# Optimization experiments

Measured on AMD Instinct MI355X. Metric: run time of the kernel, lower is better.

Reference implementation:

```python
import jax, jax.numpy as jnp
import numpy as np

N, E, F, H, C, T = 100000, 1600000, 128, 64, 8, 4

def setup_inputs() -> dict:
    key = jax.random.key(0)
    ks = jax.random.split(key, 16)
    inp = {
        'x': jax.random.normal(ks[0], (N, F), dtype=jnp.float32),
        'node_types': jax.random.randint(ks[1], (N,), 0, T, dtype=jnp.int64),
        'edge_index0': jax.random.randint(ks[2], (2, E), 0, N, dtype=jnp.int64),
        'edge_index1': jax.random.randint(ks[3], (2, E), 0, N, dtype=jnp.int64),
        # per-node-type input projections
        'W_in': jax.random.normal(ks[4], (T, F, H), dtype=jnp.float32) / np.sqrt(F),
        'b_in': jnp.zeros((T, H), dtype=jnp.float32),
        # 4 GCN convs (layer0: paths [0,0],[0,1]; layer1: paths [0,0],[1,0])
        'W_conv': jax.random.normal(ks[5], (4, H, H), dtype=jnp.float32) / np.sqrt(H),
        'b_conv': jnp.zeros((4, H), dtype=jnp.float32),
        # output attention/classifier layers
        'W1': jax.random.normal(ks[6], (H, H), dtype=jnp.float32) / np.sqrt(H),
        'b1': jnp.zeros((H,), dtype=jnp.float32),
        'W2': jax.random.normal(ks[7], (H, 1), dtype=jnp.float32) / np.sqrt(H),
        'b2': jnp.zeros((1,), dtype=jnp.float32),
        'W3': jax.random.normal(ks[8], (H, C), dtype=jnp.float32) / np.sqrt(H),
        'b3': jnp.zeros((C,), dtype=jnp.float32),
    }
    return inp


def gcn_conv(x, edge_index, W, b):
    # PyG GCNConv: add self-loops, symmetric normalization, then scatter-add.
    n = x.shape[0]
    loop = jnp.arange(n, dtype=edge_index.dtype)
    src = jnp.concatenate([edge_index[0], loop])
    dst = jnp.concatenate([edge_index[1], loop])
    deg = jax.ops.segment_sum(jnp.ones_like(dst, dtype=x.dtype), dst, num_segments=n)
    dinv = jnp.where(deg > 0, jax.lax.rsqrt(deg), 0.0)
    norm = dinv[src] * dinv[dst]            # [E+N]
    xw = x @ W                              # [N,H]
    msg = xw[src] * norm[:, None]           # [E+N,H]
    out = jax.ops.segment_sum(msg, dst, num_segments=n)
    return out + b


def reference(x, node_types, edge_index0, edge_index1,
              W_in, b_in, W_conv, b_conv, W1, b1, W2, b2, W3, b3):
    # per-node-type input linear (fixed small loop over T types)
    hid = jnp.zeros((x.shape[0], H), dtype=x.dtype)
    for t in range(T):
        ht = x @ W_in[t] + b_in[t]
        hid = jnp.where((node_types == t)[:, None], ht, hid)
    edges = [edge_index0, edge_index1]
    states = [hid]
    # layer 0: paths [state 0, adj 0], [state 0, adj 1]; layer_agg = max
    h0 = gcn_conv(states[0], edges[0], W_conv[0], b_conv[0])
    h1 = gcn_conv(states[0], edges[1], W_conv[1], b_conv[1])
    states.append(jnp.maximum(h0, h1))
    # layer 1: paths [state 0, adj 0], [state 1, adj 0]
    h2 = gcn_conv(states[0], edges[0], W_conv[2], b_conv[2])
    h3 = gcn_conv(states[1], edges[0], W_conv[3], b_conv[3])
    states.append(jnp.maximum(h2, h3))
    # LayerNorm (no affine) + gelu (torch default = exact erf form)
    tmp = states[-1]
    mu = jnp.mean(tmp, axis=-1, keepdims=True)
    var = jnp.mean(jnp.square(tmp - mu), axis=-1, keepdims=True)
    tmp = (tmp - mu) * jax.lax.rsqrt(var + 1e-5)
    hidi = jax.nn.gelu(tmp, approximate=False)
    # attention combine over (single) temp state
    attn = jax.nn.softmax(jnp.tanh(hidi @ W1 + b1) @ W2 + b2, axis=-1)  # [N,1] -> ones
    out = attn * hidi
    return out @ W3 + b3
```

## Files before the change

kernel.cpp:

```cpp
#include <hip/hip_runtime.h>
#include <hip/hip_bf16.h>
#include <math.h>


#define HID   64
#define RB    128
#define CHUNK 4096

__device__ __forceinline__ float bflo(unsigned u) { return __int_as_float((int)(u << 16)); }
__device__ __forceinline__ float bfhi(unsigned u) { return __int_as_float((int)(u & 0xFFFF0000u)); }
__device__ __forceinline__ float bf2f(ushort v) { return __int_as_float((int)(((unsigned)v) << 16)); }
__device__ __forceinline__ ushort f2bf(float f) {
    unsigned u = __float_as_uint(f);
    unsigned r = u + 0x7FFFu + ((u >> 16) & 1u);
    return (ushort)(r >> 16);
}
__device__ __forceinline__ void addw(float a[4], uint2 v, float wgt) {
    a[0] = fmaf(bflo(v.x), wgt, a[0]);
    a[1] = fmaf(bfhi(v.x), wgt, a[1]);
    a[2] = fmaf(bflo(v.y), wgt, a[2]);
    a[3] = fmaf(bfhi(v.y), wgt, a[3]);
}
__device__ __forceinline__ void addu(float a[4], uint2 v) {
    a[0] += bflo(v.x); a[1] += bfhi(v.x);
    a[2] += bflo(v.y); a[3] += bfhi(v.y);
}

__global__ void zeroRow(unsigned* __restrict__ ghz, unsigned* __restrict__ s1z,
                        float* __restrict__ dinv0, float* __restrict__ dinv1, int N) {
    int tid = threadIdx.x;
    if (tid < 32) { ghz[tid] = 0u; s1z[tid] = 0u; }
    if (tid == 0) { dinv0[N] = 0.0f; dinv1[N] = 0.0f; }
}

__global__ void histA(const int* __restrict__ dst0, const int* __restrict__ dst1,
                      int E, unsigned M, int* __restrict__ bcnt) {
    __shared__ int h[2 * RB];
    for (int i = threadIdx.x; i < 2 * RB; i += blockDim.x) h[i] = 0;
    __syncthreads();
    int stride = gridDim.x * blockDim.x;
    for (int i = blockIdx.x * blockDim.x + threadIdx.x; i < E; i += stride) {
        atomicAdd(&h[__umulhi((unsigned)dst0[i], M)], 1);
        atomicAdd(&h[RB + __umulhi((unsigned)dst1[i], M)], 1);
    }
    __syncthreads();
    for (int i = threadIdx.x; i < 2 * RB; i += blockDim.x)
        if (h[i]) atomicAdd(&bcnt[i], h[i]);
}

__global__ void scanA(const int* __restrict__ bcnt, int* __restrict__ bbase,
                      int* __restrict__ bcur) {
    __shared__ int t[2 * RB];
    int tid = threadIdx.x;
    int orig = bcnt[tid];
    t[tid] = orig;
    __syncthreads();
    int list = tid >> 7, r = tid & (RB - 1);
    for (int o = 1; o < RB; o <<= 1) {
        int u = (r >= o) ? t[tid - o] : 0;
        __syncthreads();
        t[tid] += u;
        __syncthreads();
    }
    int incl = t[tid];
    int excl = incl - orig;
    bbase[list * (RB + 1) + r] = excl;
    bcur[tid] = excl;
    if (r == RB - 1) bbase[list * (RB + 1) + RB] = incl;
}

__global__ void __launch_bounds__(256) partB(const int* __restrict__ e0,
                                             const int* __restrict__ e1,
                                             int E, int BW, unsigned M,
                                             int* __restrict__ bcur_all,
                                             unsigned* __restrict__ arena_all) {
    __shared__ int hist[RB], scn[RB], lbase[RB], cur[RB], gbase[RB];
    __shared__ uint2 buf[CHUNK];
    int half = gridDim.x >> 1;
    int list = (blockIdx.x >= half) ? 1 : 0;
    const int* src = list ? e1 : e0;
    const int* dst = src + E;
    int* bcur = bcur_all + list * RB;
    unsigned* arena = arena_all + (size_t)list * E;
    int blk = blockIdx.x - list * half;
    int tid = threadIdx.x;

    for (int c0 = blk * CHUNK; c0 < E; c0 += half * CHUNK) {
        int cn = min(CHUNK, E - c0);
        for (int i = tid; i < RB; i += 256) hist[i] = 0;
        __syncthreads();
        unsigned ls[16], ld[16];
        #pragma unroll
        for (int k = 0; k < 16; ++k) {
            int j = k * 256 + tid;
            ld[k] = 0xFFFFFFFFu; ls[k] = 0;
            if (j < cn) {
                ls[k] = (unsigned)src[c0 + j];
                ld[k] = (unsigned)dst[c0 + j];
                atomicAdd(&hist[__umulhi(ld[k], M)], 1);
            }
        }
        __syncthreads();
        if (tid < RB) scn[tid] = hist[tid];
        __syncthreads();
        for (int o = 1; o < RB; o <<= 1) {
            int u = (tid < RB && tid >= o) ? scn[tid - o] : 0;
            __syncthreads();
            if (tid < RB) scn[tid] += u;
            __syncthreads();
        }
        if (tid < RB) {
            int ex = scn[tid] - hist[tid];
            lbase[tid] = ex;
            cur[tid]   = ex;
            gbase[tid] = hist[tid] ? atomicAdd(&bcur[tid], hist[tid]) : 0;
        }
        __syncthreads();
        #pragma unroll
        for (int k = 0; k < 16; ++k) {
            if (ld[k] != 0xFFFFFFFFu) {
                int b = __umulhi(ld[k], M);
                int slot = atomicAdd(&cur[b], 1);
                buf[slot] = make_uint2(ls[k], ld[k]);
            }
        }
        __syncthreads();
        for (int i = tid; i < cn; i += 256) {
            uint2 p = buf[i];
            int b = __umulhi(p.y, M);
            arena[gbase[b] + (i - lbase[b])] = (p.x << 10) | (p.y - (unsigned)(b * BW));
        }
        __syncthreads();
    }
}

__global__ void __launch_bounds__(1024) buildC(const unsigned* __restrict__ arena_all,
                                               const int* __restrict__ bbase,
                                               int E, int N, int BW,
                                               int* __restrict__ csr0p, int* __restrict__ csr1p,
                                               unsigned* __restrict__ offp0, unsigned* __restrict__ offp1,
                                               float* __restrict__ dinv0, float* __restrict__ dinv1) {
    __shared__ int degl[800], scn[800], cur[800];
    int list = blockIdx.x >> 7, rb = blockIdx.x & (RB - 1);
    const unsigned* arena = arena_all + (size_t)list * E;
    int* csr = list ? csr1p : csr0p;
    unsigned* offp = list ? offp1 : offp0;
    float* dinv = list ? dinv1 : dinv0;
    int base = bbase[list * (RB + 1) + rb];
    int end  = bbase[list * (RB + 1) + rb + 1];
    int csrb = base + 16 * BW * rb;
    int nbase = rb * BW;
    int nn = min(BW, N - nbase);
    if (nn <= 0) return;
    int tid = threadIdx.x;
    for (int i = tid; i < nn; i += 1024) degl[i] = 0;
    __syncthreads();
    for (int j = base + tid; j < end; j += 1024)
        atomicAdd(&degl[arena[j] & 1023u], 1);
    __syncthreads();
    int d = (tid < nn) ? degl[tid] : 0;
    int dp = d ? ((d + 15) & ~15) : 0;
    if (tid < nn) scn[tid] = dp;
    __syncthreads();
    for (int o = 1; o < nn; o <<= 1) {
        int u = (tid < nn && tid >= o) ? scn[tid - o] : 0;
        __syncthreads();
        if (tid < nn) scn[tid] += u;
        __syncthreads();
    }
    if (tid < nn) {
        int ex = scn[tid] - dp;
        cur[tid] = ex;
        offp[nbase + tid] = (unsigned)(csrb + ex) | ((unsigned)(dp >> 4) << 25);
        dinv[nbase + tid] = rsqrtf((float)(d + 1));
        for (int j = ex + d; j < ex + dp; ++j) csr[csrb + j] = N;
    }
    __syncthreads();
    for (int j = base + tid; j < end; j += 1024) {
        unsigned p = arena[j];
        int loc = atomicAdd(&cur[p & 1023u], 1);
        csr[csrb + loc] = (int)(p >> 10);
    }
}

__global__ void input_proj(const float* __restrict__ x, const int* __restrict__ types,
                           const float* __restrict__ W_in, const float* __restrict__ b_in,
                           ushort* __restrict__ gh, int N, int F) {
    __shared__ float xs[4 * 128];
    int tid = threadIdx.x;
    int w = tid >> 6, h = tid & 63;
    int n0 = blockIdx.x * 4;
    for (int i = tid; i < 4 * F; i += 256) {
        int nn = n0 + i / F;
        xs[i] = (nn < N) ? x[(size_t)nn * F + (i % F)] : 0.0f;
    }
    __syncthreads();
    int n = n0 + w;
    if (n >= N) return;
    int t = types[n];
    const float* W = W_in + (size_t)t * F * HID;
    float acc = b_in[t * HID + h];
    const float* xr = xs + w * F;
    #pragma unroll 16
    for (int f = 0; f < F; ++f)
        acc = fmaf(xr[f], W[(size_t)f * HID + h], acc);
    gh[(size_t)n * HID + h] = f2bf(acc);
}

__device__ __forceinline__ void gatherW(const uint2* __restrict__ GH,
                                        const float* __restrict__ dv,
                                        const int* __restrict__ csr,
                                        unsigned wword, int q, int fl, float a[4]) {
    int base = (int)(wword & 0x1FFFFFFu);
    int it = (int)(wword >> 25);
    if (it == 0) return;
    const int* cp = csr + base;
    int ia = cp[q], ib = cp[4 + q], ic = cp[8 + q], id = cp[12 + q];
    while (true) {
        uint2 va = GH[(size_t)ia * 16 + fl];
        uint2 vb = GH[(size_t)ib * 16 + fl];
        uint2 vc = GH[(size_t)ic * 16 + fl];
        uint2 vd = GH[(size_t)id * 16 + fl];
        float wa = dv[ia], wb = dv[ib], wc = dv[ic], wd = dv[id];
        --it; cp += 16;
        int na = 0, nb = 0, nc = 0, nd = 0;
        if (it > 0) { na = cp[q]; nb = cp[4 + q]; nc = cp[8 + q]; nd = cp[12 + q]; }
        addw(a, va, wa); addw(a, vb, wb); addw(a, vc, wc); addw(a, vd, wd);
        if (it == 0) break;
        ia = na; ib = nb; ic = nc; id = nd;
    }
}

__device__ __forceinline__ void gatherU(const uint2* __restrict__ GH,
                                        const int* __restrict__ csr,
                                        unsigned wword, int q, int fl, float a[4]) {
    int base = (int)(wword & 0x1FFFFFFu);
    int it = (int)(wword >> 25);
    if (it == 0) return;
    const int* cp = csr + base;
    int ia = cp[q], ib = cp[4 + q], ic = cp[8 + q], id = cp[12 + q];
    while (true) {
        uint2 va = GH[(size_t)ia * 16 + fl];
        uint2 vb = GH[(size_t)ib * 16 + fl];
        uint2 vc = GH[(size_t)ic * 16 + fl];
        uint2 vd = GH[(size_t)id * 16 + fl];
        --it; cp += 16;
        int na = 0, nb = 0, nc = 0, nd = 0;
        if (it > 0) { na = cp[q]; nb = cp[4 + q]; nc = cp[8 + q]; nd = cp[12 + q]; }
        addu(a, va); addu(a, vb); addu(a, vc); addu(a, vd);
        if (it == 0) break;
        ia = na; ib = nb; ic = nc; id = nd;
    }
}

__global__ void __launch_bounds__(512) gatherL1(
        const ushort* __restrict__ gh,
        const unsigned* __restrict__ offp0, const int* __restrict__ csr0p,
        const float* __restrict__ dinv0,
        const unsigned* __restrict__ offp1, const int* __restrict__ csr1p,
        const float* __restrict__ dinv1,
        const float* __restrict__ W_conv, const float* __restrict__ b_conv,
        unsigned* __restrict__ a0g, ushort* __restrict__ s1g, int N) {
    __shared__ float Ws[2 * HID * HID];
    __shared__ float l0[8][HID], l1[8][HID];
    int tid = threadIdx.x;
    for (int i = tid; i < 2 * HID * HID; i += 512) Ws[i] = W_conv[i];
    __syncthreads();
    int w = tid >> 6, lane = tid & 63;
    int q = lane >> 4, fl = lane & 15;
    int n = blockIdx.x * 8 + w;
    if (n >= N) return;
    const uint2* GH = (const uint2*)gh;
    float d0 = dinv0[n], d1 = dinv1[n];
    float a0[4] = {0, 0, 0, 0}, a1[4] = {0, 0, 0, 0};
    if (q == 0) {
        uint2 sv = GH[(size_t)n * 16 + fl];
        float f0 = bflo(sv.x), f1 = bfhi(sv.x), f2 = bflo(sv.y), f3 = bfhi(sv.y);
        a0[0] = f0 * d0; a0[1] = f1 * d0; a0[2] = f2 * d0; a0[3] = f3 * d0;
        a1[0] = f0 * d1; a1[1] = f1 * d1; a1[2] = f2 * d1; a1[3] = f3 * d1;
    }
    gatherW(GH, dinv0, csr0p, offp0[n], q, fl, a0);
    gatherW(GH, dinv1, csr1p, offp1[n], q, fl, a1);
    #pragma unroll
    for (int k = 0; k < 4; ++k) {
        a0[k] += __shfl_xor(a0[k], 16, 64);
        a0[k] += __shfl_xor(a0[k], 32, 64);
        a1[k] += __shfl_xor(a1[k], 16, 64);
        a1[k] += __shfl_xor(a1[k], 32, 64);
        a0[k] *= d0;
        a1[k] *= d1;
    }
    if (q == 0) {
        *(float4*)&l0[w][fl * 4] = make_float4(a0[0], a0[1], a0[2], a0[3]);
        *(float4*)&l1[w][fl * 4] = make_float4(a1[0], a1[1], a1[2], a1[3]);
        uint2 pk;
        pk.x = (unsigned)f2bf(a0[0]) | ((unsigned)f2bf(a0[1]) << 16);
        pk.y = (unsigned)f2bf(a0[2]) | ((unsigned)f2bf(a0[3]) << 16);
        ((uint2*)a0g)[(size_t)n * 16 + fl] = pk;
    }
    int h = lane;
    float m0 = b_conv[h];
    float m1 = b_conv[HID + h];
    #pragma unroll 8
    for (int k = 0; k < HID; ++k) {
        m0 = fmaf(l0[w][k], Ws[k * HID + h], m0);
        m1 = fmaf(l1[w][k], Ws[HID * HID + k * HID + h], m1);
    }
    s1g[(size_t)n * HID + h] = f2bf(fmaxf(m0, m1) * d0);
}

__global__ void __launch_bounds__(512) gatherL2(
        const unsigned* __restrict__ a0g, const ushort* __restrict__ s1g,
        const unsigned* __restrict__ offp0, const int* __restrict__ csr0p,
        const float* __restrict__ dinv0,
        const float* __restrict__ W_conv, const float* __restrict__ b_conv,
        const float* __restrict__ W3, const float* __restrict__ b3,
        float* __restrict__ out, int N) {
    __shared__ float Ws[2 * HID * HID];
    __shared__ float W3s[HID * 8];
    __shared__ float l2[8][HID], l3[8][HID], gs[8][HID];
    int tid = threadIdx.x;
    for (int i = tid; i < 2 * HID * HID; i += 512) Ws[i] = W_conv[2 * HID * HID + i];
    if (tid < HID * 8) W3s[tid] = W3[tid];
    __syncthreads();
    int w = tid >> 6, lane = tid & 63;
    int q = lane >> 4, fl = lane & 15;
    int n = blockIdx.x * 8 + w;
    if (n >= N) return;
    const uint2* S = (const uint2*)s1g;
    float d0 = dinv0[n];
    float a[4] = {0, 0, 0, 0};
    if (q == 0) {
        uint2 sv = S[(size_t)n * 16 + fl];
        a[0] = bflo(sv.x); a[1] = bfhi(sv.x);
        a[2] = bflo(sv.y); a[3] = bfhi(sv.y);
        uint2 av = ((const uint2*)a0g)[(size_t)n * 16 + fl];
        *(float4*)&l2[w][fl * 4] = make_float4(bflo(av.x), bfhi(av.x), bflo(av.y), bfhi(av.y));
    }
    gatherU(S, csr0p, offp0[n], q, fl, a);
    #pragma unroll
    for (int k = 0; k < 4; ++k) {
        a[k] += __shfl_xor(a[k], 16, 64);
        a[k] += __shfl_xor(a[k], 32, 64);
        a[k] *= d0;
    }
    if (q == 0)
        *(float4*)&l3[w][fl * 4] = make_float4(a[0], a[1], a[2], a[3]);
    int h = lane;
    float m2 = b_conv[2 * HID + h];
    float m3 = b_conv[3 * HID + h];
    #pragma unroll 8
    for (int k = 0; k < HID; ++k) {
        m2 = fmaf(l2[w][k], Ws[k * HID + h], m2);
        m3 = fmaf(l3[w][k], Ws[HID * HID + k * HID + h], m3);
    }
    float s2 = fmaxf(m2, m3);
    float sum = s2;
    #pragma unroll
    for (int off = 32; off; off >>= 1) sum += __shfl_xor(sum, off, 64);
    float mu = sum * (1.0f / 64.0f);
    float dv = s2 - mu;
    float v = dv * dv;
    #pragma unroll
    for (int off = 32; off; off >>= 1) v += __shfl_xor(v, off, 64);
    float xn = dv * rsqrtf(v * (1.0f / 64.0f) + 1e-5f);
    float g = 0.5f * xn * (1.0f + erff(xn * 0.70710678118654752f));
    gs[w][h] = g;
    if (h < 8) {
        float acc = b3[h];
        #pragma unroll 8
        for (int k = 0; k < HID; ++k)
            acc = fmaf(gs[w][k], W3s[k * 8 + h], acc);
        out[(size_t)n * 8 + h] = acc;
    }
}

extern "C" void kernel_launch(void* const* d_in, const int* in_sizes, int n_in,
                              void* d_out, int out_size, void* d_ws, size_t ws_size,
                              hipStream_t stream) {
    const float* x          = (const float*)d_in[0];
    const int*   node_types = (const int*)d_in[1];
    const int*   e0         = (const int*)d_in[2];
    const int*   e1         = (const int*)d_in[3];
    const float* W_in       = (const float*)d_in[4];
    const float* b_in       = (const float*)d_in[5];
    const float* W_conv     = (const float*)d_in[6];
    const float* b_conv     = (const float*)d_in[7];
    const float* W3         = (const float*)d_in[12];
    const float* b3         = (const float*)d_in[13];
    float* out = (float*)d_out;

    int N = in_sizes[1];
    int F = in_sizes[0] / N;
    int E = in_sizes[2] / 2;
    int BW = (N + RB - 1) / RB;
    unsigned M = (unsigned)(0x100000000ULL / (unsigned long long)BW) + 1u;
    size_t EP = (size_t)E + 16 * (size_t)BW * RB + 64;

    unsigned* ws32 = (unsigned*)d_ws;
    int*      bcnt  = (int*)ws32;
    int*      bbase = bcnt + 2 * RB;
    int*      bcur  = bbase + 2 * (RB + 1);
    unsigned* offp0 = (unsigned*)(bcur + 2 * RB + 6);
    unsigned* offp1 = offp0 + (N + 1);
    float*    dinv0 = (float*)(offp1 + (N + 1));
    float*    dinv1 = dinv0 + (N + 1);
    int*      csr0p = (int*)(dinv1 + (N + 1));
    int*      csr1p = csr0p + EP;
    ushort*   gh    = (ushort*)(csr1p + EP);
    ushort*   s1g   = gh + (size_t)(N + 1) * HID;
    unsigned* a0g   = (unsigned*)(s1g + (size_t)(N + 1) * HID);
    unsigned* arena = a0g;

    (void)hipMemsetAsync(bcnt, 0, 2 * RB * sizeof(int), stream);
    zeroRow<<<1, 64, 0, stream>>>((unsigned*)(gh + (size_t)N * HID),
                                  (unsigned*)(s1g + (size_t)N * HID), dinv0, dinv1, N);
    histA<<<1024, 256, 0, stream>>>(e0 + E, e1 + E, E, M, bcnt);
    scanA<<<1, 256, 0, stream>>>(bcnt, bbase, bcur);
    partB<<<256, 256, 0, stream>>>(e0, e1, E, BW, M, bcur, arena);
    buildC<<<2 * RB, 1024, 0, stream>>>(arena, bbase, E, N, BW,
                                        csr0p, csr1p, offp0, offp1, dinv0, dinv1);
    input_proj<<<(N + 3) / 4, 256, 0, stream>>>(x, node_types, W_in, b_in, gh, N, F);
    gatherL1<<<(N + 7) / 8, 512, 0, stream>>>(gh, offp0, csr0p, dinv0, offp1, csr1p, dinv1,
                                              W_conv, b_conv, a0g, s1g, N);
    gatherL2<<<(N + 7) / 8, 512, 0, stream>>>(a0g, s1g, offp0, csr0p, dinv0,
                                              W_conv, b_conv, W3, b3, out, N);
}
```

Baseline: 484.0 us.

## Process two nodes per wavefront in gatherL2 with interleaved neighbor gathers

gatherL2 now gives each 64-lane wavefront two destination nodes instead of one. Their CSR neighbor gathers are interleaved so eight row loads are in flight per iteration, and the Ws/W3 shared-memory reads are reused across both nodes in the small matmuls. Block count is halved and the shared buffers are doubled. This raises memory-level parallelism and halves per-node weight reads, at the cost of more registers, load imbalance between the paired nodes' degrees, and the loss of the software prefetch of the next index batch.

```diff
diff --git a/kernel.cpp b/kernel.cpp
--- a/kernel.cpp
+++ b/kernel.cpp
@@ -231,25 +231,48 @@
     }
 }
 
-__device__ __forceinline__ void gatherU(const uint2* __restrict__ GH,
-                                        const int* __restrict__ csr,
-                                        unsigned wword, int q, int fl, float a[4]) {
-    int base = (int)(wword & 0x1FFFFFFu);
-    int it = (int)(wword >> 25);
-    if (it == 0) return;
-    const int* cp = csr + base;
-    int ia = cp[q], ib = cp[4 + q], ic = cp[8 + q], id = cp[12 + q];
-    while (true) {
-        uint2 va = GH[(size_t)ia * 16 + fl];
-        uint2 vb = GH[(size_t)ib * 16 + fl];
-        uint2 vc = GH[(size_t)ic * 16 + fl];
-        uint2 vd = GH[(size_t)id * 16 + fl];
-        --it; cp += 16;
-        int na = 0, nb = 0, nc = 0, nd = 0;
-        if (it > 0) { na = cp[q]; nb = cp[4 + q]; nc = cp[8 + q]; nd = cp[12 + q]; }
-        addu(a, va); addu(a, vb); addu(a, vc); addu(a, vd);
-        if (it == 0) break;
-        ia = na; ib = nb; ic = nc; id = nd;
+__device__ __forceinline__ void gatherU2(const uint2* __restrict__ GH,
+                                         const int* __restrict__ csr,
+                                         unsigned wA, unsigned wB,
+                                         int q, int fl, float aA[4], float aB[4]) {
+    int baseA = (int)(wA & 0x1FFFFFFu), itA = (int)(wA >> 25);
+    int baseB = (int)(wB & 0x1FFFFFFu), itB = (int)(wB >> 25);
+    const int* cpA = csr + baseA;
+    const int* cpB = csr + baseB;
+    int c = min(itA, itB);
+    for (int i = 0; i < c; ++i) {
+        int a0 = cpA[q], a1 = cpA[4 + q], a2 = cpA[8 + q], a3 = cpA[12 + q];
+        int b0 = cpB[q], b1 = cpB[4 + q], b2 = cpB[8 + q], b3 = cpB[12 + q];
+        uint2 vA0 = GH[(size_t)a0 * 16 + fl];
+        uint2 vA1 = GH[(size_t)a1 * 16 + fl];
+        uint2 vA2 = GH[(size_t)a2 * 16 + fl];
+        uint2 vA3 = GH[(size_t)a3 * 16 + fl];
+        uint2 vB0 = GH[(size_t)b0 * 16 + fl];
+        uint2 vB1 = GH[(size_t)b1 * 16 + fl];
+        uint2 vB2 = GH[(size_t)b2 * 16 + fl];
+        uint2 vB3 = GH[(size_t)b3 * 16 + fl];
+        addu(aA, vA0); addu(aA, vA1); addu(aA, vA2); addu(aA, vA3);
+        addu(aB, vB0); addu(aB, vB1); addu(aB, vB2); addu(aB, vB3);
+        cpA += 16; cpB += 16;
+    }
+    itA -= c; itB -= c;
+    for (; itA > 0; --itA) {
+        int a0 = cpA[q], a1 = cpA[4 + q], a2 = cpA[8 + q], a3 = cpA[12 + q];
+        uint2 v0 = GH[(size_t)a0 * 16 + fl];
+        uint2 v1 = GH[(size_t)a1 * 16 + fl];
+        uint2 v2 = GH[(size_t)a2 * 16 + fl];
+        uint2 v3 = GH[(size_t)a3 * 16 + fl];
+        addu(aA, v0); addu(aA, v1); addu(aA, v2); addu(aA, v3);
+        cpA += 16;
+    }
+    for (; itB > 0; --itB) {
+        int b0 = cpB[q], b1 = cpB[4 + q], b2 = cpB[8 + q], b3 = cpB[12 + q];
+        uint2 v0 = GH[(size_t)b0 * 16 + fl];
+        uint2 v1 = GH[(size_t)b1 * 16 + fl];
+        uint2 v2 = GH[(size_t)b2 * 16 + fl];
+        uint2 v3 = GH[(size_t)b3 * 16 + fl];
+        addu(aB, v0); addu(aB, v1); addu(aB, v2); addu(aB, v3);
+        cpB += 16;
     }
 }
 
@@ -318,60 +341,95 @@
         float* __restrict__ out, int N) {
     __shared__ float Ws[2 * HID * HID];
     __shared__ float W3s[HID * 8];
-    __shared__ float l2[8][HID], l3[8][HID], gs[8][HID];
+    __shared__ float l2[16][HID], l3[16][HID], gs[16][HID];
     int tid = threadIdx.x;
     for (int i = tid; i < 2 * HID * HID; i += 512) Ws[i] = W_conv[2 * HID * HID + i];
     if (tid < HID * 8) W3s[tid] = W3[tid];
     __syncthreads();
     int w = tid >> 6, lane = tid & 63;
     int q = lane >> 4, fl = lane & 15;
-    int n = blockIdx.x * 8 + w;
-    if (n >= N) return;
+    int nA = blockIdx.x * 16 + 2 * w;
+    int nB = nA + 1;
+    if (nA >= N) return;
+    bool hasB = (nB < N);
     const uint2* S = (const uint2*)s1g;
-    float d0 = dinv0[n];
-    float a[4] = {0, 0, 0, 0};
+    float d0A = dinv0[nA];
+    float d0B = hasB ? dinv0[nB] : 0.0f;
+    float aA[4] = {0, 0, 0, 0}, aB[4] = {0, 0, 0, 0};
     if (q == 0) {
-        uint2 sv = S[(size_t)n * 16 + fl];
-        a[0] = bflo(sv.x); a[1] = bfhi(sv.x);
-        a[2] = bflo(sv.y); a[3] = bfhi(sv.y);
-        uint2 av = ((const uint2*)a0g)[(size_t)n * 16 + fl];
-        *(float4*)&l2[w][fl * 4] = make_float4(bflo(av.x), bfhi(av.x), bflo(av.y), bfhi(av.y));
-    }
-    gatherU(S, csr0p, offp0[n], q, fl, a);
+        uint2 sv = S[(size_t)nA * 16 + fl];
+        aA[0] = bflo(sv.x); aA[1] = bfhi(sv.x);
+        aA[2] = bflo(sv.y); aA[3] = bfhi(sv.y);
+        uint2 av = ((const uint2*)a0g)[(size_t)nA * 16 + fl];
+        *(float4*)&l2[2 * w][fl * 4] = make_float4(bflo(av.x), bfhi(av.x), bflo(av.y), bfhi(av.y));
+    }
+    if (q == 1 && hasB) {
+        uint2 sv = S[(size_t)nB * 16 + fl];
+        aB[0] = bflo(sv.x); aB[1] = bfhi(sv.x);
+        aB[2] = bflo(sv.y); aB[3] = bfhi(sv.y);
+        uint2 av = ((const uint2*)a0g)[(size_t)nB * 16 + fl];
+        *(float4*)&l2[2 * w + 1][fl * 4] = make_float4(bflo(av.x), bfhi(av.x), bflo(av.y), bfhi(av.y));
+    }
+    unsigned wwA = offp0[nA];
+    unsigned wwB = hasB ? offp0[nB] : 0u;
+    gatherU2(S, csr0p, wwA, wwB, q, fl, aA, aB);
     #pragma unroll
     for (int k = 0; k < 4; ++k) {
-        a[k] += __shfl_xor(a[k], 16, 64);
-        a[k] += __shfl_xor(a[k], 32, 64);
-        a[k] *= d0;
+        aA[k] += __shfl_xor(aA[k], 16, 64);
+        aA[k] += __shfl_xor(aA[k], 32, 64);
+        aB[k] += __shfl_xor(aB[k], 16, 64);
+        aB[k] += __shfl_xor(aB[k], 32, 64);
+        aA[k] *= d0A;
+        aB[k] *= d0B;
     }
     if (q == 0)
-        *(float4*)&l3[w][fl * 4] = make_float4(a[0], a[1], a[2], a[3]);
+        *(float4*)&l3[2 * w][fl * 4] = make_float4(aA[0], aA[1], aA[2], aA[3]);
+    if (q == 1 && hasB)
+        *(float4*)&l3[2 * w + 1][fl * 4] = make_float4(aB[0], aB[1], aB[2], aB[3]);
     int h = lane;
-    float m2 = b_conv[2 * HID + h];
-    float m3 = b_conv[3 * HID + h];
+    float m2A = b_conv[2 * HID + h], m3A = b_conv[3 * HID + h];
+    float m2B = m2A, m3B = m3A;
     #pragma unroll 8
     for (int k = 0; k < HID; ++k) {
-        m2 = fmaf(l2[w][k], Ws[k * HID + h], m2);
-        m3 = fmaf(l3[w][k], Ws[HID * HID + k * HID + h], m3);
-    }
-    float s2 = fmaxf(m2, m3);
-    float sum = s2;
+        float w2 = Ws[k * HID + h];
+        float w3 = Ws[HID * HID + k * HID + h];
+        m2A = fmaf(l2[2 * w][k], w2, m2A);
+        m3A = fmaf(l3[2 * w][k], w3, m3A);
+        m2B = fmaf(l2[2 * w + 1][k], w2, m2B);
+        m3B = fmaf(l3[2 * w + 1][k], w3, m3B);
+    }
+    float s2A = fmaxf(m2A, m3A);
+    float s2B = fmaxf(m2B, m3B);
+    float sumA = s2A, sumB = s2B;
     #pragma unroll
-    for (int off = 32; off; off >>= 1) sum += __shfl_xor(sum, off, 64);
-    float mu = sum * (1.0f / 64.0f);
-    float dv = s2 - mu;
-    float v = dv * dv;
+    for (int off = 32; off; off >>= 1) {
+        sumA += __shfl_xor(sumA, off, 64);
+        sumB += __shfl_xor(sumB, off, 64);
+    }
+    float muA = sumA * (1.0f / 64.0f), muB = sumB * (1.0f / 64.0f);
+    float dvA = s2A - muA, dvB = s2B - muB;
+    float vA = dvA * dvA, vB = dvB * dvB;
     #pragma unroll
-    for (int off = 32; off; off >>= 1) v += __shfl_xor(v, off, 64);
-    float xn = dv * rsqrtf(v * (1.0f / 64.0f) + 1e-5f);
-    float g = 0.5f * xn * (1.0f + erff(xn * 0.70710678118654752f));
-    gs[w][h] = g;
+    for (int off = 32; off; off >>= 1) {
+        vA += __shfl_xor(vA, off, 64);
+        vB += __shfl_xor(vB, off, 64);
+    }
+    float xnA = dvA * rsqrtf(vA * (1.0f / 64.0f) + 1e-5f);
+    float xnB = dvB * rsqrtf(vB * (1.0f / 64.0f) + 1e-5f);
+    float gA = 0.5f * xnA * (1.0f + erff(xnA * 0.70710678118654752f));
+    float gB = 0.5f * xnB * (1.0f + erff(xnB * 0.70710678118654752f));
+    gs[2 * w][h] = gA;
+    gs[2 * w + 1][h] = gB;
     if (h < 8) {
-        float acc = b3[h];
+        float accA = b3[h], accB = b3[h];
         #pragma unroll 8
-        for (int k = 0; k < HID; ++k)
-            acc = fmaf(gs[w][k], W3s[k * 8 + h], acc);
-        out[(size_t)n * 8 + h] = acc;
+        for (int k = 0; k < HID; ++k) {
+            float w3v = W3s[k * 8 + h];
+            accA = fmaf(gs[2 * w][k], w3v, accA);
+            accB = fmaf(gs[2 * w + 1][k], w3v, accB);
+        }
+        out[(size_t)nA * 8 + h] = accA;
+        if (hasB) out[(size_t)nB * 8 + h] = accB;
     }
 }
 
@@ -423,6 +481,6 @@
     input_proj<<<(N + 3) / 4, 256, 0, stream>>>(x, node_types, W_in, b_in, gh, N, F);
     gatherL1<<<(N + 7) / 8, 512, 0, stream>>>(gh, offp0, csr0p, dinv0, offp1, csr1p, dinv1,
                                               W_conv, b_conv, a0g, s1g, N);
-    gatherL2<<<(N + 7) / 8, 512, 0, stream>>>(a0g, s1g, offp0, csr0p, dinv0,
-                                              W_conv, b_conv, W3, b3, out, N);
-}
+    gatherL2<<<(N + 15) / 16, 512, 0, stream>>>(a0g, s1g, offp0, csr0p, dinv0,
+                                                W_conv, b_conv, W3, b3, out, N);
+}
```

Measured after the change: 455.8 us, median of 2. -5.8%, faster.
